# Performance work log

Hardware: AMD Instinct MI355X
Metric: run time of the kernel (lower is better)

Reference implementation:

```python
import jax, jax.numpy as jnp
import numpy as np

B, C, H, W = 4, 256, 64, 64
C8 = C // 8


def setup_inputs() -> dict:
    key = jax.random.key(0)
    ks = jax.random.split(key, 8)
    x = jax.random.normal(ks[0], (B, C, H, W), dtype=jnp.float32)
    valid = jax.random.uniform(ks[1], (B, 1, H, W), dtype=jnp.float32)
    # 1x1 conv weights (kernel_size=1 -> plain channel matmul) + biases
    Wq = jax.random.normal(ks[2], (C8, C), dtype=jnp.float32) * 0.05
    bq = jnp.zeros((C8,), dtype=jnp.float32)
    Wk = jax.random.normal(ks[3], (C8, C), dtype=jnp.float32) * 0.05
    bk = jnp.zeros((C8,), dtype=jnp.float32)
    Wv = jax.random.normal(ks[4], (C, C), dtype=jnp.float32) * 0.05
    bv = jnp.zeros((C,), dtype=jnp.float32)
    gamma = jnp.asarray(0.5, dtype=jnp.float32)  # nonzero so attention path matters
    return {"x": x, "valid": valid, "Wq": Wq, "bq": bq, "Wk": Wk, "bk": bk,
            "Wv": Wv, "bv": bv, "gamma": gamma}


def reference(x, valid, Wq, bq, Wk, bk, Wv, bv, gamma):
    b, c, h, w = x.shape
    n = h * w
    xf = x.reshape(b, c, n)                                   # [B,C,N]
    # valid is already at (H,W): nearest interpolate to same size is identity
    v = valid.reshape(b, 1, n)                                # [B,1,N]
    q = jnp.einsum('oc,bcn->bno', Wq, xf) + bq                # [B,N,C//8]
    k = jnp.einsum('oc,bcn->bon', Wk, xf) + bk[None, :, None] # [B,C//8,N]
    energy = jnp.einsum('bno,bom->bnm', q, k)                 # [B,N,N]
    attn = jax.nn.softmax(energy, axis=-1)
    va = attn * v                                             # mask columns
    scale = 1.0 / jnp.sum(va, axis=2, keepdims=True)          # per-row renorm
    sa = va * scale                                           # [B,N,N]
    pv = jnp.einsum('oc,bcn->bon', Wv, xf) + bv[None, :, None]  # [B,C,N]
    out = jnp.einsum('bon,bmn->bom', pv, sa)                  # bmm(V, A^T)
    out = out.reshape(b, c, h, w)
    return gamma * out + x, sa
```

## Files before the change

kernel.cpp:

```cpp
#include <hip/hip_runtime.h>

typedef unsigned short u16;
typedef unsigned int u32;
typedef __attribute__((ext_vector_type(8))) short short8;
typedef __attribute__((ext_vector_type(4))) float f32x4;
typedef __attribute__((ext_vector_type(2))) unsigned int u32x2;

#define BB 4
#define CC 256
#define NT 4096
#define L2E 1.4426950408889634f

__device__ __forceinline__ float b2f(u16 v) {
    union { u32 u; float f; } c; c.u = ((u32)v) << 16; return c.f;
}
__device__ __forceinline__ u16 f2b(float f) {
    union { float f; u32 u; } c; c.f = f;
    u32 u = c.u;
    return (u16)((u + 0x7fffu + ((u >> 16) & 1u)) >> 16);
}

__global__ __launch_bounds__(256) void kproj(
    const float* __restrict__ x,
    const float* __restrict__ Wq, const float* __restrict__ bq,
    const float* __restrict__ Wk, const float* __restrict__ bk,
    const float* __restrict__ Wv, const float* __restrict__ bv,
    u16* __restrict__ qh, u16* __restrict__ ql,
    u16* __restrict__ kh, u16* __restrict__ kl,
    u16* __restrict__ pvw)
{
    __shared__ __align__(16) float lA[32][68];
    __shared__ __align__(16) float lX[32][68];
    const int mt = blockIdx.x, nt = blockIdx.y, b = blockIdx.z;
    const int t = threadIdx.x;
    const int tx = t & 15, ty = t >> 4;
    const int n0 = nt * 64;

    float acc[4][4];
    #pragma unroll
    for (int i = 0; i < 4; ++i)
        #pragma unroll
        for (int j = 0; j < 4; ++j) acc[i][j] = 0.f;

    const int rA = t >> 2, kqA = (t & 3) * 8;
    const int rgA = mt * 64 + rA;
    const float* wrow;
    if (rgA < 32)      wrow = Wq + rgA * 256;
    else if (rgA < 64) wrow = Wk + (rgA - 32) * 256;
    else               wrow = Wv + (rgA - 64) * 256;
    const int kX = t >> 3, nn8 = (t & 7) * 8;
    const float* xrow = x + ((size_t)(b * CC + kX)) * NT + n0 + nn8;

    for (int k0 = 0; k0 < 256; k0 += 32) {
        f32x4 wa = *(const f32x4*)(wrow + k0 + kqA);
        f32x4 wb = *(const f32x4*)(wrow + k0 + kqA + 4);
        f32x4 xa = *(const f32x4*)(xrow + (size_t)k0 * NT);
        f32x4 xb = *(const f32x4*)(xrow + (size_t)k0 * NT + 4);
        __syncthreads();
        #pragma unroll
        for (int j = 0; j < 4; ++j) {
            lA[kqA + j    ][rA] = wa[j];
            lA[kqA + j + 4][rA] = wb[j];
        }
        *(f32x4*)&lX[kX][nn8]     = xa;
        *(f32x4*)&lX[kX][nn8 + 4] = xb;
        __syncthreads();
        #pragma unroll
        for (int k = 0; k < 32; ++k) {
            f32x4 av  = *(const f32x4*)&lA[k][ty * 4];
            f32x4 xvv = *(const f32x4*)&lX[k][tx * 4];
            #pragma unroll
            for (int i = 0; i < 4; ++i)
                #pragma unroll
                for (int j = 0; j < 4; ++j)
                    acc[i][j] = fmaf(av[i], xvv[j], acc[i][j]);
        }
    }

    #pragma unroll
    for (int i = 0; i < 4; ++i) {
        const int rg = mt * 64 + ty * 4 + i;
        float bias;
        if (rg < 32)      bias = bq[rg];
        else if (rg < 64) bias = bk[rg - 32];
        else              bias = bv[rg - 64];
        #pragma unroll
        for (int j = 0; j < 4; ++j) {
            const int n = n0 + tx * 4 + j;
            const float val = acc[i][j] + bias;
            const u16 h = f2b(val);
            const u16 l = f2b(val - b2f(h));
            if (rg < 32) {
                const size_t idx = ((size_t)(b * NT + n)) * 32 + rg;
                qh[idx] = h; ql[idx] = l;
            } else if (rg < 64) {
                const size_t idx = ((size_t)(b * NT + n)) * 32 + (rg - 32);
                kh[idx] = h; kl[idx] = l;
            } else {
                pvw[((size_t)b * CC + (rg - 64)) * NT + n] = f2b(val);
            }
        }
    }
}

__global__ __launch_bounds__(256) void kattn(
    const u16* __restrict__ qh, const u16* __restrict__ ql,
    const u16* __restrict__ kh, const u16* __restrict__ kl,
    const float* __restrict__ valid, float* __restrict__ sa)
{
    const int b    = blockIdx.y;
    const int lane = threadIdx.x & 63;
    const int wv   = threadIdx.x >> 6;
    const int r0   = (blockIdx.x * 4 + wv) * 16;
    const int quad = lane >> 4, l16 = lane & 15;

    const size_t abase = ((size_t)(b * NT + r0 + l16)) * 32 + quad * 8;
    const short8 aqh = *(const short8*)(qh + abase);
    const short8 aql = *(const short8*)(ql + abase);
    const size_t kb = (size_t)b * NT * 32 + (size_t)l16 * 32 + quad * 8;
    const float* vb = valid + b * NT + l16;
    const f32x4 zero = {0.f, 0.f, 0.f, 0.f};

    float sacc[4] = {0.f, 0.f, 0.f, 0.f};
    for (int ct = 0; ct < 256; ++ct) {
        short8 bh = *(const short8*)(kh + kb + (size_t)ct * 512);
        short8 bl = *(const short8*)(kl + kb + (size_t)ct * 512);
        float vcol = vb[ct * 16];
        f32x4 d = __builtin_amdgcn_mfma_f32_16x16x32_bf16(aqh, bh, zero, 0, 0, 0);
        d = __builtin_amdgcn_mfma_f32_16x16x32_bf16(aql, bh, d, 0, 0, 0);
        d = __builtin_amdgcn_mfma_f32_16x16x32_bf16(aqh, bl, d, 0, 0, 0);
        #pragma unroll
        for (int i = 0; i < 4; ++i)
            sacc[i] += vcol * exp2f(fminf(d[i], 60.f) * L2E);
    }
    #pragma unroll
    for (int i = 0; i < 4; ++i) {
        #pragma unroll
        for (int off = 1; off < 16; off <<= 1)
            sacc[i] += __shfl_xor(sacc[i], off, 64);
        sacc[i] = 1.0f / sacc[i];
    }
    for (int ct = 0; ct < 256; ++ct) {
        short8 bh = *(const short8*)(kh + kb + (size_t)ct * 512);
        short8 bl = *(const short8*)(kl + kb + (size_t)ct * 512);
        float vcol = vb[ct * 16];
        f32x4 d = __builtin_amdgcn_mfma_f32_16x16x32_bf16(aqh, bh, zero, 0, 0, 0);
        d = __builtin_amdgcn_mfma_f32_16x16x32_bf16(aql, bh, d, 0, 0, 0);
        d = __builtin_amdgcn_mfma_f32_16x16x32_bf16(aqh, bl, d, 0, 0, 0);
        #pragma unroll
        for (int i = 0; i < 4; ++i) {
            float val = vcol * exp2f(fminf(d[i], 60.f) * L2E) * sacc[i];
            sa[((size_t)(b * NT + r0 + quad * 4 + i)) * NT + ct * 16 + l16] = val;
        }
    }
}

__global__ __launch_bounds__(512) void kout(
    const u16* __restrict__ pvw, const float* __restrict__ sa,
    const float* __restrict__ x, const float* __restrict__ gamma,
    float* __restrict__ outp)
{
    __shared__ __align__(16) u16 lB[32][72];
    const int b    = blockIdx.y;
    const int m0   = blockIdx.x * 32;
    const int t    = threadIdx.x;
    const int lane = t & 63;
    const int wv   = t >> 6;
    const int c0   = wv * 32;
    const int quad = lane >> 4, l16 = lane & 15;

    const u16* a0p = pvw + ((size_t)(b * CC + c0 + l16)) * NT + quad * 8;
    const u16* a1p = a0p + (size_t)16 * NT;
    const int sm = t >> 4, sk = (t & 15) * 4;
    const float* sap = sa + ((size_t)(b * NT + m0 + sm)) * NT + sk;

    f32x4 acc00 = {0,0,0,0}, acc01 = {0,0,0,0}, acc10 = {0,0,0,0}, acc11 = {0,0,0,0};

    for (int k0 = 0; k0 < NT; k0 += 64) {
        f32x4 sv = *(const f32x4*)(sap + k0);
        __syncthreads();
        u32x2 packed;
        packed[0] = (u32)f2b(sv[0]) | ((u32)f2b(sv[1]) << 16);
        packed[1] = (u32)f2b(sv[2]) | ((u32)f2b(sv[3]) << 16);
        *(u32x2*)&lB[sm][sk] = packed;
        __syncthreads();
        #pragma unroll
        for (int half = 0; half < 64; half += 32) {
            short8 a0 = *(const short8*)(a0p + k0 + half);
            short8 a1 = *(const short8*)(a1p + k0 + half);
            short8 b0 = *(const short8*)&lB[l16     ][half + quad * 8];
            short8 b1 = *(const short8*)&lB[16 + l16][half + quad * 8];
            acc00 = __builtin_amdgcn_mfma_f32_16x16x32_bf16(a0, b0, acc00, 0, 0, 0);
            acc01 = __builtin_amdgcn_mfma_f32_16x16x32_bf16(a0, b1, acc01, 0, 0, 0);
            acc10 = __builtin_amdgcn_mfma_f32_16x16x32_bf16(a1, b0, acc10, 0, 0, 0);
            acc11 = __builtin_amdgcn_mfma_f32_16x16x32_bf16(a1, b1, acc11, 0, 0, 0);
        }
    }

    const float g = gamma[0];
    #pragma unroll
    for (int ai = 0; ai < 2; ++ai) {
        #pragma unroll
        for (int bi = 0; bi < 2; ++bi) {
            f32x4 acc = (ai == 0) ? ((bi == 0) ? acc00 : acc01)
                                  : ((bi == 0) ? acc10 : acc11);
            #pragma unroll
            for (int i = 0; i < 4; ++i) {
                const int c = c0 + ai * 16 + quad * 4 + i;
                const int m = m0 + bi * 16 + l16;
                const size_t idx = ((size_t)(b * CC + c)) * NT + m;
                outp[idx] = g * acc[i] + x[idx];
            }
        }
    }
}

extern "C" void kernel_launch(void* const* d_in, const int* in_sizes, int n_in,
                              void* d_out, int out_size, void* d_ws, size_t ws_size,
                              hipStream_t stream)
{
    const float* x     = (const float*)d_in[0];
    const float* valid = (const float*)d_in[1];
    const float* Wq    = (const float*)d_in[2];
    const float* bq    = (const float*)d_in[3];
    const float* Wk    = (const float*)d_in[4];
    const float* bk    = (const float*)d_in[5];
    const float* Wv    = (const float*)d_in[6];
    const float* bv    = (const float*)d_in[7];
    const float* gamma = (const float*)d_in[8];

    float* outp = (float*)d_out;
    float* sa   = outp + (size_t)BB * CC * NT;

    u16* qh  = (u16*)d_ws;
    u16* ql  = qh + (size_t)BB * NT * 32;
    u16* kh  = ql + (size_t)BB * NT * 32;
    u16* kl  = kh + (size_t)BB * NT * 32;
    u16* pvw = kl + (size_t)BB * NT * 32;

    kproj<<<dim3(5, 64, BB), 256, 0, stream>>>(x, Wq, bq, Wk, bk, Wv, bv,
                                               qh, ql, kh, kl, pvw);
    kattn<<<dim3(64, BB), 256, 0, stream>>>(qh, ql, kh, kl, valid, sa);
    kout<<<dim3(128, BB), 512, 0, stream>>>(pvw, sa, x, gamma, outp);
}
```

Baseline: 629.5 us.

## Use split-bf16 MFMA projection, LDS-staged K tiles in attention, direct sa loads in output

The projection kernel is rebuilt around bf16 MFMA with hi/lo split operands, fed by two new prep kernels that split the weights and transpose and split x. The attention kernel now stages 128-column K tiles and the valid mask in LDS, prefetching the next tile, so all four waves share them. The output kernel drops its LDS staging and packs fp32 sa to bf16 in registers with a cheap perm-based round. This adds two extra launches and more workspace traffic, and the new packing rounds differently from round-to-nearest-even.

```diff
diff --git a/kernel.cpp b/kernel.cpp
--- a/kernel.cpp
+++ b/kernel.cpp
@@ -19,85 +19,113 @@
     u32 u = c.u;
     return (u16)((u + 0x7fffu + ((u >> 16) & 1u)) >> 16);
 }
-
-__global__ __launch_bounds__(256) void kproj(
-    const float* __restrict__ x,
-    const float* __restrict__ Wq, const float* __restrict__ bq,
-    const float* __restrict__ Wk, const float* __restrict__ bk,
-    const float* __restrict__ Wv, const float* __restrict__ bv,
+#define MFMA16(A, B, C) __builtin_amdgcn_mfma_f32_16x16x32_bf16(A, B, C, 0, 0, 0)
+
+__device__ __forceinline__ short8 pack8(f32x4 a, f32x4 b) {
+    union { f32x4 f; u32 u[4]; } A, Bu; A.f = a; Bu.f = b;
+    union { u32 u[4]; short8 s; } R;
+    R.u[0] = __builtin_amdgcn_perm(A.u[1]  + 0x8000u, A.u[0]  + 0x8000u, 0x07060302u);
+    R.u[1] = __builtin_amdgcn_perm(A.u[3]  + 0x8000u, A.u[2]  + 0x8000u, 0x07060302u);
+    R.u[2] = __builtin_amdgcn_perm(Bu.u[1] + 0x8000u, Bu.u[0] + 0x8000u, 0x07060302u);
+    R.u[3] = __builtin_amdgcn_perm(Bu.u[3] + 0x8000u, Bu.u[2] + 0x8000u, 0x07060302u);
+    return R.s;
+}
+
+__global__ __launch_bounds__(256) void kwsplit(
+    const float* __restrict__ Wq, const float* __restrict__ Wk,
+    const float* __restrict__ Wv, u16* __restrict__ wh, u16* __restrict__ wl)
+{
+    const int e = blockIdx.x * 256 + threadIdx.x;
+    const int m = e >> 8, k = e & 255;
+    float v;
+    if (m < 32)      v = Wq[m * 256 + k];
+    else if (m < 64) v = Wk[(m - 32) * 256 + k];
+    else             v = Wv[(m - 64) * 256 + k];
+    const u16 h = f2b(v);
+    wh[e] = h; wl[e] = f2b(v - b2f(h));
+}
+
+__global__ __launch_bounds__(256) void kcast(
+    const float* __restrict__ x, u16* __restrict__ xth, u16* __restrict__ xtl)
+{
+    __shared__ float lT[32][33];
+    const int b = blockIdx.z, c0 = blockIdx.y * 32, n0 = blockIdx.x * 32;
+    const int t = threadIdx.x;
+    const int lr = t >> 3, lc4 = (t & 7) * 4;
+    f32x4 v = *(const f32x4*)(x + ((size_t)(b * CC + c0 + lr)) * NT + n0 + lc4);
+    #pragma unroll
+    for (int j = 0; j < 4; ++j) lT[lr][lc4 + j] = v[j];
+    __syncthreads();
+    u16 h[4], l[4];
+    #pragma unroll
+    for (int j = 0; j < 4; ++j) {
+        float f = lT[lc4 + j][lr];
+        h[j] = f2b(f); l[j] = f2b(f - b2f(h[j]));
+    }
+    const size_t o = ((size_t)(b * NT + n0 + lr)) * CC + c0 + lc4;
+    u32x2 ph, pl;
+    ph[0] = (u32)h[0] | ((u32)h[1] << 16); ph[1] = (u32)h[2] | ((u32)h[3] << 16);
+    pl[0] = (u32)l[0] | ((u32)l[1] << 16); pl[1] = (u32)l[2] | ((u32)l[3] << 16);
+    *(u32x2*)(xth + o) = ph;
+    *(u32x2*)(xtl + o) = pl;
+}
+
+__global__ __launch_bounds__(64) void kproj(
+    const u16* __restrict__ wh, const u16* __restrict__ wl,
+    const u16* __restrict__ xth, const u16* __restrict__ xtl,
+    const float* __restrict__ bq, const float* __restrict__ bk,
+    const float* __restrict__ bv,
     u16* __restrict__ qh, u16* __restrict__ ql,
-    u16* __restrict__ kh, u16* __restrict__ kl,
-    u16* __restrict__ pvw)
-{
-    __shared__ __align__(16) float lA[32][68];
-    __shared__ __align__(16) float lX[32][68];
-    const int mt = blockIdx.x, nt = blockIdx.y, b = blockIdx.z;
-    const int t = threadIdx.x;
-    const int tx = t & 15, ty = t >> 4;
-    const int n0 = nt * 64;
-
-    float acc[4][4];
-    #pragma unroll
-    for (int i = 0; i < 4; ++i)
-        #pragma unroll
-        for (int j = 0; j < 4; ++j) acc[i][j] = 0.f;
-
-    const int rA = t >> 2, kqA = (t & 3) * 8;
-    const int rgA = mt * 64 + rA;
-    const float* wrow;
-    if (rgA < 32)      wrow = Wq + rgA * 256;
-    else if (rgA < 64) wrow = Wk + (rgA - 32) * 256;
-    else               wrow = Wv + (rgA - 64) * 256;
-    const int kX = t >> 3, nn8 = (t & 7) * 8;
-    const float* xrow = x + ((size_t)(b * CC + kX)) * NT + n0 + nn8;
-
+    u16* __restrict__ kh, u16* __restrict__ kl, u16* __restrict__ pvw)
+{
+    const int b = blockIdx.z, m0 = blockIdx.y * 32, n0 = blockIdx.x * 32;
+    const int lane = threadIdx.x, quad = lane >> 4, l16 = lane & 15;
+
+    const u16* awh0 = wh + (m0 + l16) * 256 + quad * 8;
+    const u16* awl0 = wl + (m0 + l16) * 256 + quad * 8;
+    const size_t xoff = ((size_t)(b * NT + n0 + l16)) * CC + quad * 8;
+    const u16* bxh0 = xth + xoff;
+    const u16* bxl0 = xtl + xoff;
+
+    f32x4 a00 = {0,0,0,0}, a01 = {0,0,0,0}, a10 = {0,0,0,0}, a11 = {0,0,0,0};
+    #pragma unroll 2
     for (int k0 = 0; k0 < 256; k0 += 32) {
-        f32x4 wa = *(const f32x4*)(wrow + k0 + kqA);
-        f32x4 wb = *(const f32x4*)(wrow + k0 + kqA + 4);
-        f32x4 xa = *(const f32x4*)(xrow + (size_t)k0 * NT);
-        f32x4 xb = *(const f32x4*)(xrow + (size_t)k0 * NT + 4);
-        __syncthreads();
-        #pragma unroll
-        for (int j = 0; j < 4; ++j) {
-            lA[kqA + j    ][rA] = wa[j];
-            lA[kqA + j + 4][rA] = wb[j];
-        }
-        *(f32x4*)&lX[kX][nn8]     = xa;
-        *(f32x4*)&lX[kX][nn8 + 4] = xb;
-        __syncthreads();
-        #pragma unroll
-        for (int k = 0; k < 32; ++k) {
-            f32x4 av  = *(const f32x4*)&lA[k][ty * 4];
-            f32x4 xvv = *(const f32x4*)&lX[k][tx * 4];
+        short8 Ah0 = *(const short8*)(awh0 + k0);
+        short8 Ah1 = *(const short8*)(awh0 + 16 * 256 + k0);
+        short8 Al0 = *(const short8*)(awl0 + k0);
+        short8 Al1 = *(const short8*)(awl0 + 16 * 256 + k0);
+        short8 Bh0 = *(const short8*)(bxh0 + k0);
+        short8 Bh1 = *(const short8*)(bxh0 + 16 * CC + k0);
+        short8 Bl0 = *(const short8*)(bxl0 + k0);
+        short8 Bl1 = *(const short8*)(bxl0 + 16 * CC + k0);
+        a00 = MFMA16(Ah0, Bh0, a00); a00 = MFMA16(Al0, Bh0, a00); a00 = MFMA16(Ah0, Bl0, a00);
+        a01 = MFMA16(Ah0, Bh1, a01); a01 = MFMA16(Al0, Bh1, a01); a01 = MFMA16(Ah0, Bl1, a01);
+        a10 = MFMA16(Ah1, Bh0, a10); a10 = MFMA16(Al1, Bh0, a10); a10 = MFMA16(Ah1, Bl0, a10);
+        a11 = MFMA16(Ah1, Bh1, a11); a11 = MFMA16(Al1, Bh1, a11); a11 = MFMA16(Ah1, Bl1, a11);
+    }
+
+    #pragma unroll
+    for (int i = 0; i < 2; ++i) {
+        #pragma unroll
+        for (int j = 0; j < 2; ++j) {
+            f32x4 acc = (i == 0) ? ((j == 0) ? a00 : a01) : ((j == 0) ? a10 : a11);
             #pragma unroll
-            for (int i = 0; i < 4; ++i)
-                #pragma unroll
-                for (int j = 0; j < 4; ++j)
-                    acc[i][j] = fmaf(av[i], xvv[j], acc[i][j]);
-        }
-    }
-
-    #pragma unroll
-    for (int i = 0; i < 4; ++i) {
-        const int rg = mt * 64 + ty * 4 + i;
-        float bias;
-        if (rg < 32)      bias = bq[rg];
-        else if (rg < 64) bias = bk[rg - 32];
-        else              bias = bv[rg - 64];
-        #pragma unroll
-        for (int j = 0; j < 4; ++j) {
-            const int n = n0 + tx * 4 + j;
-            const float val = acc[i][j] + bias;
-            const u16 h = f2b(val);
-            const u16 l = f2b(val - b2f(h));
-            if (rg < 32) {
-                const size_t idx = ((size_t)(b * NT + n)) * 32 + rg;
-                qh[idx] = h; ql[idx] = l;
-            } else if (rg < 64) {
-                const size_t idx = ((size_t)(b * NT + n)) * 32 + (rg - 32);
-                kh[idx] = h; kl[idx] = l;
-            } else {
-                pvw[((size_t)b * CC + (rg - 64)) * NT + n] = f2b(val);
+            for (int r = 0; r < 4; ++r) {
+                const int m = m0 + i * 16 + quad * 4 + r;
+                const int n = n0 + j * 16 + l16;
+                const float bias = (m < 32) ? bq[m] : (m < 64) ? bk[m - 32] : bv[m - 64];
+                const float val = acc[r] + bias;
+                if (m < 32) {
+                    const size_t idx = ((size_t)(b * NT + n)) * 32 + m;
+                    const u16 h = f2b(val);
+                    qh[idx] = h; ql[idx] = f2b(val - b2f(h));
+                } else if (m < 64) {
+                    const size_t idx = ((size_t)(b * NT + n)) * 32 + (m - 32);
+                    const u16 h = f2b(val);
+                    kh[idx] = h; kl[idx] = f2b(val - b2f(h));
+                } else {
+                    pvw[((size_t)(b * CC + m - 64)) * NT + n] = f2b(val);
+                }
             }
         }
     }
@@ -108,30 +136,56 @@
     const u16* __restrict__ kh, const u16* __restrict__ kl,
     const float* __restrict__ valid, float* __restrict__ sa)
 {
-    const int b    = blockIdx.y;
-    const int lane = threadIdx.x & 63;
-    const int wv   = threadIdx.x >> 6;
-    const int r0   = (blockIdx.x * 4 + wv) * 16;
+    __shared__ __align__(16) u16 lKh[128][40];
+    __shared__ __align__(16) u16 lKl[128][40];
+    __shared__ float lV[128];
+    const int b = blockIdx.y;
+    const int t = threadIdx.x;
+    const int lane = t & 63, wv = t >> 6;
     const int quad = lane >> 4, l16 = lane & 15;
+    const int r0 = blockIdx.x * 64 + wv * 16;
 
     const size_t abase = ((size_t)(b * NT + r0 + l16)) * 32 + quad * 8;
     const short8 aqh = *(const short8*)(qh + abase);
     const short8 aql = *(const short8*)(ql + abase);
-    const size_t kb = (size_t)b * NT * 32 + (size_t)l16 * 32 + quad * 8;
-    const float* vb = valid + b * NT + l16;
+
+    const int scol = t >> 1, skb = (t & 1) * 16;
+    const u16* khp = kh + ((size_t)(b * NT + scol)) * 32 + skb;
+    const u16* klp = kl + ((size_t)(b * NT + scol)) * 32 + skb;
+    const float* vp = valid + b * NT;
     const f32x4 zero = {0.f, 0.f, 0.f, 0.f};
 
+    short8 h0, h1, g0, g1; float vv;
+    h0 = *(const short8*)(khp); h1 = *(const short8*)(khp + 8);
+    g0 = *(const short8*)(klp); g1 = *(const short8*)(klp + 8);
+    vv = (t < 128) ? vp[t] : 0.f;
+
     float sacc[4] = {0.f, 0.f, 0.f, 0.f};
-    for (int ct = 0; ct < 256; ++ct) {
-        short8 bh = *(const short8*)(kh + kb + (size_t)ct * 512);
-        short8 bl = *(const short8*)(kl + kb + (size_t)ct * 512);
-        float vcol = vb[ct * 16];
-        f32x4 d = __builtin_amdgcn_mfma_f32_16x16x32_bf16(aqh, bh, zero, 0, 0, 0);
-        d = __builtin_amdgcn_mfma_f32_16x16x32_bf16(aql, bh, d, 0, 0, 0);
-        d = __builtin_amdgcn_mfma_f32_16x16x32_bf16(aqh, bl, d, 0, 0, 0);
-        #pragma unroll
-        for (int i = 0; i < 4; ++i)
-            sacc[i] += vcol * exp2f(fminf(d[i], 60.f) * L2E);
+    for (int ct = 0; ct < 32; ++ct) {
+        __syncthreads();
+        *(short8*)&lKh[scol][skb] = h0; *(short8*)&lKh[scol][skb + 8] = h1;
+        *(short8*)&lKl[scol][skb] = g0; *(short8*)&lKl[scol][skb + 8] = g1;
+        if (t < 128) lV[t] = vv;
+        __syncthreads();
+        if (ct < 31) {
+            const u16* p1 = khp + (size_t)(ct + 1) * 128 * 32;
+            const u16* p2 = klp + (size_t)(ct + 1) * 128 * 32;
+            h0 = *(const short8*)(p1); h1 = *(const short8*)(p1 + 8);
+            g0 = *(const short8*)(p2); g1 = *(const short8*)(p2 + 8);
+            if (t < 128) vv = vp[(ct + 1) * 128 + t];
+        }
+        #pragma unroll
+        for (int s = 0; s < 8; ++s) {
+            short8 bh = *(const short8*)&lKh[s * 16 + l16][quad * 8];
+            short8 bl = *(const short8*)&lKl[s * 16 + l16][quad * 8];
+            f32x4 d = MFMA16(aqh, bh, zero);
+            d = MFMA16(aql, bh, d);
+            d = MFMA16(aqh, bl, d);
+            const float vc = lV[s * 16 + l16];
+            #pragma unroll
+            for (int i = 0; i < 4; ++i)
+                sacc[i] += vc * exp2f(fminf(d[i], 60.f) * L2E);
+        }
     }
     #pragma unroll
     for (int i = 0; i < 4; ++i) {
@@ -140,17 +194,36 @@
             sacc[i] += __shfl_xor(sacc[i], off, 64);
         sacc[i] = 1.0f / sacc[i];
     }
-    for (int ct = 0; ct < 256; ++ct) {
-        short8 bh = *(const short8*)(kh + kb + (size_t)ct * 512);
-        short8 bl = *(const short8*)(kl + kb + (size_t)ct * 512);
-        float vcol = vb[ct * 16];
-        f32x4 d = __builtin_amdgcn_mfma_f32_16x16x32_bf16(aqh, bh, zero, 0, 0, 0);
-        d = __builtin_amdgcn_mfma_f32_16x16x32_bf16(aql, bh, d, 0, 0, 0);
-        d = __builtin_amdgcn_mfma_f32_16x16x32_bf16(aqh, bl, d, 0, 0, 0);
-        #pragma unroll
-        for (int i = 0; i < 4; ++i) {
-            float val = vcol * exp2f(fminf(d[i], 60.f) * L2E) * sacc[i];
-            sa[((size_t)(b * NT + r0 + quad * 4 + i)) * NT + ct * 16 + l16] = val;
+    h0 = *(const short8*)(khp); h1 = *(const short8*)(khp + 8);
+    g0 = *(const short8*)(klp); g1 = *(const short8*)(klp + 8);
+    vv = (t < 128) ? vp[t] : 0.f;
+    for (int ct = 0; ct < 32; ++ct) {
+        __syncthreads();
+        *(short8*)&lKh[scol][skb] = h0; *(short8*)&lKh[scol][skb + 8] = h1;
+        *(short8*)&lKl[scol][skb] = g0; *(short8*)&lKl[scol][skb + 8] = g1;
+        if (t < 128) lV[t] = vv;
+        __syncthreads();
+        if (ct < 31) {
+            const u16* p1 = khp + (size_t)(ct + 1) * 128 * 32;
+            const u16* p2 = klp + (size_t)(ct + 1) * 128 * 32;
+            h0 = *(const short8*)(p1); h1 = *(const short8*)(p1 + 8);
+            g0 = *(const short8*)(p2); g1 = *(const short8*)(p2 + 8);
+            if (t < 128) vv = vp[(ct + 1) * 128 + t];
+        }
+        #pragma unroll
+        for (int s = 0; s < 8; ++s) {
+            short8 bh = *(const short8*)&lKh[s * 16 + l16][quad * 8];
+            short8 bl = *(const short8*)&lKl[s * 16 + l16][quad * 8];
+            f32x4 d = MFMA16(aqh, bh, zero);
+            d = MFMA16(aql, bh, d);
+            d = MFMA16(aqh, bl, d);
+            const float vc = lV[s * 16 + l16];
+            const int col = ct * 128 + s * 16 + l16;
+            #pragma unroll
+            for (int i = 0; i < 4; ++i) {
+                const float val = vc * exp2f(fminf(d[i], 60.f) * L2E) * sacc[i];
+                sa[((size_t)(b * NT + r0 + quad * 4 + i)) * NT + col] = val;
+            }
         }
     }
 }
@@ -160,41 +233,28 @@
     const float* __restrict__ x, const float* __restrict__ gamma,
     float* __restrict__ outp)
 {
-    __shared__ __align__(16) u16 lB[32][72];
-    const int b    = blockIdx.y;
-    const int m0   = blockIdx.x * 32;
-    const int t    = threadIdx.x;
-    const int lane = t & 63;
-    const int wv   = t >> 6;
-    const int c0   = wv * 32;
-    const int quad = lane >> 4, l16 = lane & 15;
+    const int b = blockIdx.y, m0 = blockIdx.x * 32;
+    const int t = threadIdx.x, lane = t & 63, wv = t >> 6;
+    const int c0 = wv * 32, quad = lane >> 4, l16 = lane & 15;
 
     const u16* a0p = pvw + ((size_t)(b * CC + c0 + l16)) * NT + quad * 8;
     const u16* a1p = a0p + (size_t)16 * NT;
-    const int sm = t >> 4, sk = (t & 15) * 4;
-    const float* sap = sa + ((size_t)(b * NT + m0 + sm)) * NT + sk;
+    const float* b0p = sa + ((size_t)(b * NT + m0 + l16)) * NT + quad * 8;
+    const float* b1p = b0p + (size_t)16 * NT;
 
     f32x4 acc00 = {0,0,0,0}, acc01 = {0,0,0,0}, acc10 = {0,0,0,0}, acc11 = {0,0,0,0};
-
-    for (int k0 = 0; k0 < NT; k0 += 64) {
-        f32x4 sv = *(const f32x4*)(sap + k0);
-        __syncthreads();
-        u32x2 packed;
-        packed[0] = (u32)f2b(sv[0]) | ((u32)f2b(sv[1]) << 16);
-        packed[1] = (u32)f2b(sv[2]) | ((u32)f2b(sv[3]) << 16);
-        *(u32x2*)&lB[sm][sk] = packed;
-        __syncthreads();
-        #pragma unroll
-        for (int half = 0; half < 64; half += 32) {
-            short8 a0 = *(const short8*)(a0p + k0 + half);
-            short8 a1 = *(const short8*)(a1p + k0 + half);
-            short8 b0 = *(const short8*)&lB[l16     ][half + quad * 8];
-            short8 b1 = *(const short8*)&lB[16 + l16][half + quad * 8];
-            acc00 = __builtin_amdgcn_mfma_f32_16x16x32_bf16(a0, b0, acc00, 0, 0, 0);
-            acc01 = __builtin_amdgcn_mfma_f32_16x16x32_bf16(a0, b1, acc01, 0, 0, 0);
-            acc10 = __builtin_amdgcn_mfma_f32_16x16x32_bf16(a1, b0, acc10, 0, 0, 0);
-            acc11 = __builtin_amdgcn_mfma_f32_16x16x32_bf16(a1, b1, acc11, 0, 0, 0);
-        }
+    #pragma unroll 2
+    for (int k0 = 0; k0 < NT; k0 += 32) {
+        short8 a0 = *(const short8*)(a0p + k0);
+        short8 a1 = *(const short8*)(a1p + k0);
+        f32x4 s00 = *(const f32x4*)(b0p + k0), s01 = *(const f32x4*)(b0p + k0 + 4);
+        f32x4 s10 = *(const f32x4*)(b1p + k0), s11 = *(const f32x4*)(b1p + k0 + 4);
+        short8 bf0 = pack8(s00, s01);
+        short8 bf1 = pack8(s10, s11);
+        acc00 = MFMA16(a0, bf0, acc00);
+        acc01 = MFMA16(a0, bf1, acc01);
+        acc10 = MFMA16(a1, bf0, acc10);
+        acc11 = MFMA16(a1, bf1, acc11);
     }
 
     const float g = gamma[0];
@@ -233,13 +293,19 @@
     float* sa   = outp + (size_t)BB * CC * NT;
 
     u16* qh  = (u16*)d_ws;
-    u16* ql  = qh + (size_t)BB * NT * 32;
-    u16* kh  = ql + (size_t)BB * NT * 32;
-    u16* kl  = kh + (size_t)BB * NT * 32;
-    u16* pvw = kl + (size_t)BB * NT * 32;
-
-    kproj<<<dim3(5, 64, BB), 256, 0, stream>>>(x, Wq, bq, Wk, bk, Wv, bv,
-                                               qh, ql, kh, kl, pvw);
+    u16* ql  = qh  + (size_t)BB * NT * 32;
+    u16* kh  = ql  + (size_t)BB * NT * 32;
+    u16* kl  = kh  + (size_t)BB * NT * 32;
+    u16* pvw = kl  + (size_t)BB * NT * 32;
+    u16* xth = pvw + (size_t)BB * CC * NT;
+    u16* xtl = xth + (size_t)BB * NT * CC;
+    u16* wh  = xtl + (size_t)BB * NT * CC;
+    u16* wl  = wh  + (size_t)320 * 256;
+
+    kwsplit<<<dim3(320), 256, 0, stream>>>(Wq, Wk, Wv, wh, wl);
+    kcast<<<dim3(128, 8, BB), 256, 0, stream>>>(x, xth, xtl);
+    kproj<<<dim3(128, 10, BB), 64, 0, stream>>>(wh, wl, xth, xtl, bq, bk, bv,
+                                                qh, ql, kh, kl, pvw);
     kattn<<<dim3(64, BB), 256, 0, stream>>>(qh, ql, kh, kl, valid, sa);
     kout<<<dim3(128, BB), 512, 0, stream>>>(pvw, sa, x, gamma, outp);
 }
```

Result: slower. 776.9 us (+23.4%).
